# Optimization experiments

Measured on AMD Instinct MI355X. Metric: run time of the kernel, lower is better.

The kernel has to match this reference:

```python
import jax, jax.numpy as jnp
import numpy as np

HID, INTER, DK = 768, 1536, 128
NEG_INF = 1.0e12
LOG512 = float(np.log(512.0))


def setup_inputs() -> dict:
    key = jax.random.key(0)
    k1, k2, k3 = jax.random.split(key, 3)
    B, S = 4, 2048
    hidden_states = jax.random.normal(k1, (B, S, HID), dtype=jnp.float32)
    attention_mask = jnp.ones((B, S), dtype=jnp.int32)
    # i_dense: hidden -> 2*INTER + DK (no bias); o_dense: INTER -> hidden (no bias)
    Wi = jax.random.normal(k2, (HID, 2 * INTER + DK), dtype=jnp.float32) * (HID ** -0.5)
    Wo = jax.random.normal(k3, (INTER, HID), dtype=jnp.float32) * (INTER ** -0.5)
    q_gamma = jnp.ones((DK,), dtype=jnp.float32)  # ScaleOffset scale, offset=False
    k_gamma = jnp.ones((DK,), dtype=jnp.float32)
    return {"hidden_states": hidden_states, "Wi": Wi, "Wo": Wo,
            "q_gamma": q_gamma, "k_gamma": k_gamma,
            "attention_mask": attention_mask}


def reference(hidden_states, Wi, Wo, q_gamma, k_gamma, attention_mask):
    # i_dense + swish, then split into u, v, qk
    x = jax.nn.silu(jnp.einsum('bsh,ho->bso', hidden_states, Wi))
    u = x[..., :INTER]
    v = x[..., INTER:2 * INTER]
    qk = x[..., 2 * INTER:]
    q = qk * q_gamma
    k = qk * k_gamma
    # single-head attention scores
    a = jnp.einsum('bmd,bnd->bmn', q, k) / (DK ** 0.5)
    mask = attention_mask[:, None, :]  # [B,1,N]
    a = jnp.where(mask == 0, -NEG_INF, a)
    l = jnp.sum(attention_mask, axis=-1, keepdims=True)[:, :, None].astype(a.dtype)  # [B,1,1]
    # softmax_plus: softmax(a * log(l) / log(512))
    A = jax.nn.softmax(a * jnp.log(l) / LOG512, axis=-1)
    # dropout inactive in eval mode
    o = jnp.einsum('bmi,ih->bmh', u * jnp.einsum('bmn,bnd->bmd', A, v), Wo)
    return o
```

## Files before the change

### kernel.cpp

```cpp
#include <hip/hip_runtime.h>
#include <hip/hip_bf16.h>
#include <math.h>

#define BATCH 4
#define SEQ   2048
#define HID   768
#define INTER 1536
#define DK    128
#define NTOT  3200
#define NTOTP 3328
#define MROWS 8192
#define LN512 6.2383246250395075f

typedef _Float16 half8   __attribute__((ext_vector_type(8)));
typedef _Float16 half4   __attribute__((ext_vector_type(4)));
typedef float    floatx4 __attribute__((ext_vector_type(4)));
typedef float    floatx16 __attribute__((ext_vector_type(16)));

typedef const __attribute__((address_space(1))) unsigned int* gas1_t;
typedef __attribute__((address_space(3))) unsigned int* las3_t;

static __device__ __forceinline__ void load16(const _Float16* g, _Float16* l) {
    __builtin_amdgcn_global_load_lds((gas1_t)g, (las3_t)l, 16, 0, 0);
}
#define WAIT_VM(N)    asm volatile("s_waitcnt vmcnt(" #N ")" ::: "memory")
#define WAIT_LGKM0()  asm volatile("s_waitcnt lgkmcnt(0)" ::: "memory")
#define BARRIER_RAW() asm volatile("s_barrier" ::: "memory")
#define GLOAD16(dst, ptr) \
    asm volatile("global_load_dwordx4 %0, %1, off" : "=v"(dst) : "v"(ptr) : "memory")

__global__ __launch_bounds__(256) void prep_kernel(
    const float* __restrict__ H, _Float16* __restrict__ Hb,
    const float* __restrict__ Wi, _Float16* __restrict__ WiT,
    const float* __restrict__ Wo, _Float16* __restrict__ WoT,
    const int* __restrict__ mask, float* __restrict__ scales)
{
    __shared__ _Float16 tile[32][33];
    __shared__ int sh[256];
    const int bid = blockIdx.x, tid = threadIdx.x;
    if (bid < 3072) {
        const int i = (bid * 256 + tid) * 8;
        float4 a = *reinterpret_cast<const float4*>(H + i);
        float4 b = *reinterpret_cast<const float4*>(H + i + 4);
        half8 h = {(_Float16)a.x, (_Float16)a.y, (_Float16)a.z, (_Float16)a.w,
                   (_Float16)b.x, (_Float16)b.y, (_Float16)b.z, (_Float16)b.w};
        *reinterpret_cast<half8*>(Hb + i) = h;
    } else if (bid < 3072 + 2496) {
        const int l = bid - 3072;
        const int c0 = (l % 104) * 32, r0 = (l / 104) * 32;
        const int tx = tid & 31, ty = tid >> 5;
#pragma unroll
        for (int j = 0; j < 32; j += 8)
            tile[tx][ty + j] = (c0 + tx < NTOT)
                ? (_Float16)Wi[(size_t)(r0 + ty + j) * NTOT + c0 + tx]
                : (_Float16)0.0f;
        __syncthreads();
#pragma unroll
        for (int j = 0; j < 32; j += 8)
            WiT[(size_t)(c0 + ty + j) * HID + r0 + tx] = tile[ty + j][tx];
    } else if (bid < 3072 + 2496 + 1152) {
        const int l = bid - (3072 + 2496);
        const int c0 = (l % 24) * 32, r0 = (l / 24) * 32;
        const int tx = tid & 31, ty = tid >> 5;
#pragma unroll
        for (int j = 0; j < 32; j += 8)
            tile[tx][ty + j] = (_Float16)Wo[(size_t)(r0 + ty + j) * HID + c0 + tx];
        __syncthreads();
#pragma unroll
        for (int j = 0; j < 32; j += 8)
            WoT[(size_t)(c0 + ty + j) * INTER + r0 + tx] = tile[ty + j][tx];
    } else {
        const int b = bid - (3072 + 2496 + 1152);
        int s = 0;
        for (int i = tid; i < SEQ; i += 256) s += mask[b * SEQ + i];
        sh[tid] = s;
        __syncthreads();
        for (int off = 128; off > 0; off >>= 1) {
            if (tid < off) sh[tid] += sh[tid + off];
            __syncthreads();
        }
        if (tid == 0) scales[b] = logf((float)sh[0]) / LN512;
    }
}

struct TileCtx {
    int tid, wave, lane, quad, l16, l31, half, wm, wn, c0, c1;
};
static __device__ __forceinline__ TileCtx make_ctx() {
    TileCtx t;
    t.tid = threadIdx.x;
    t.wave = t.tid >> 6; t.lane = t.tid & 63;
    t.quad = t.lane >> 4; t.l16 = t.lane & 15;
    t.l31 = t.lane & 31;  t.half = t.lane >> 5;
    t.wm = (t.wave & 1) * 64;
    t.wn = (t.wave >> 1) * 64;
    t.c0 = t.tid;
    t.c1 = t.tid + 256;
    return t;
}

static __device__ __forceinline__ void gemm_mainloop_3s32(
    const TileCtx& t,
    const _Float16* __restrict__ Ag, int lda,
    const _Float16* __restrict__ Bg, int ldb,
    int K, _Float16* smem, floatx16 acc[2][2])
{
    const int r0i = t.c0 >> 2, s0 = (((r0i >> 1) ^ (r0i >> 3)) & 3);
    const int r1i = t.c1 >> 2, s1 = (((r1i >> 1) ^ (r1i >> 3)) & 3);
    const int ak0 = ((t.c0 & 3) ^ s0) * 8;
    const int ak1 = ((t.c1 & 3) ^ s1) * 8;
    const _Float16* a0 = Ag + (size_t)r0i * lda + ak0;
    const _Float16* a1 = Ag + (size_t)r1i * lda + ak1;
    const _Float16* b0 = Bg + (size_t)r0i * ldb + ak0;
    const _Float16* b1 = Bg + (size_t)r1i * ldb + ak1;
    _Float16* Asl = smem + t.c0 * 8;
    _Float16* Bsl = smem + 12288 + t.c0 * 8;
    const int nIter = K >> 5;

    const int fsw = ((t.l31 >> 1) ^ (t.l31 >> 3)) & 3;

    load16(a0, Asl);        load16(a1, Asl + 2048);
    load16(b0, Bsl);        load16(b1, Bsl + 2048);
    if (nIter > 1) {
        load16(a0 + 32, Asl + 4096); load16(a1 + 32, Asl + 6144);
        load16(b0 + 32, Bsl + 4096); load16(b1 + 32, Bsl + 6144);
    }

    int sc = 0, sp = 2;
    for (int k = 0; k < nIter; ++k) {
        if (k + 1 < nIter) { WAIT_VM(4); } else { WAIT_VM(0); }
        BARRIER_RAW();
        if (k + 2 < nIter) {
            const int off = sp * 4096;
            const int k0 = (k + 2) << 5;
            load16(a0 + k0, Asl + off); load16(a1 + k0, Asl + off + 2048);
            load16(b0 + k0, Bsl + off); load16(b1 + k0, Bsl + off + 2048);
        }
        const _Float16* Ab = smem + sc * 4096;
        const _Float16* Bb = smem + 12288 + sc * 4096;
        half8 af[2][2], bf[2][2];
#pragma unroll
        for (int mt = 0; mt < 2; ++mt)
#pragma unroll
            for (int h = 0; h < 2; ++h)
                af[mt][h] = *reinterpret_cast<const half8*>(
                    Ab + (t.wm + mt * 32 + t.l31) * 32 + (((h * 2 + t.half) ^ fsw) * 8));
#pragma unroll
        for (int nt = 0; nt < 2; ++nt)
#pragma unroll
            for (int h = 0; h < 2; ++h)
                bf[nt][h] = *reinterpret_cast<const half8*>(
                    Bb + (t.wn + nt * 32 + t.l31) * 32 + (((h * 2 + t.half) ^ fsw) * 8));
#pragma unroll
        for (int h = 0; h < 2; ++h)
#pragma unroll
            for (int mt = 0; mt < 2; ++mt)
#pragma unroll
                for (int nt = 0; nt < 2; ++nt)
                    acc[mt][nt] = __builtin_amdgcn_mfma_f32_32x32x16_f16(af[mt][h], bf[nt][h], acc[mt][nt], 0, 0, 0);
        WAIT_LGKM0();
        sc = (sc == 2) ? 0 : sc + 1;
        sp = (sp == 2) ? 0 : sp + 1;
    }
}

__global__ __launch_bounds__(512, 2) void gemm1_kernel(
    const _Float16* __restrict__ Hb, const _Float16* __restrict__ WiT,
    const float* __restrict__ qg, const float* __restrict__ kg,
    _Float16* __restrict__ u, _Float16* __restrict__ vT,
    _Float16* __restrict__ q, _Float16* __restrict__ k)
{
    __shared__ _Float16 smem[65536];
    const int tid = threadIdx.x;
    const int lane = tid & 63, wave = tid >> 6;
    const int quad = lane >> 4, l16 = lane & 15;
    const int wm = wave >> 2, wn = wave & 3;

    const int f = blockIdx.x;
    const int xcd = f & 7, i = f >> 3;
    const int m0 = (xcd * 4 + (i & 3)) * 256;
    const int ntile = i >> 2;
    const int n0 = ntile * 256;

    const _Float16* Ag = Hb  + (size_t)m0 * HID;
    const _Float16* Bg = WiT + (size_t)n0 * HID;

    const int rA = tid >> 2;
    const int csw = ((tid & 3) ^ ((rA >> 1) & 3)) * 8;
    const _Float16* pa0 = Ag + (size_t)rA * HID + csw;
    const _Float16* pa1 = pa0 + (size_t)128 * HID;
    const _Float16* pb0 = Bg + (size_t)rA * HID + csw;
    const _Float16* pb1 = pb0 + (size_t)128 * HID;

    const int sw8 = (l16 >> 1) & 3;
    const int qs  = (quad ^ sw8) * 8;
    const int aoff = (wm * 128 + l16) * 32 + qs;
    const int boff = 8192 + (wn * 64 + l16) * 32 + qs;

    floatx4 acc[8][4] = {};

    const int nKt = HID / 32;

#pragma unroll
    for (int pt = 0; pt < 3; ++pt) {
        _Float16* ld = smem + pt * 16384 + tid * 8;
        const int ko = pt * 32;
        load16(pa0 + ko, ld);
        load16(pa1 + ko, ld + 4096);
        load16(pb0 + ko, ld + 8192);
        load16(pb1 + ko, ld + 12288);
    }
    WAIT_VM(8);
    BARRIER_RAW();

    for (int t = 0; t < nKt; ++t) {
        const _Float16* sl = smem + (t & 3) * 16384;
        if (t + 3 < nKt) {
            _Float16* ld = smem + ((t + 3) & 3) * 16384 + tid * 8;
            const int ko = (t + 3) * 32;
            load16(pa0 + ko, ld);        load16(pa1 + ko, ld + 4096);
            load16(pb0 + ko, ld + 8192); load16(pb1 + ko, ld + 12288);
        }
        half8 af[8], bf[4];
#pragma unroll
        for (int mt = 0; mt < 8; ++mt)
            af[mt] = *reinterpret_cast<const half8*>(sl + aoff + mt * 512);
#pragma unroll
        for (int nt = 0; nt < 4; ++nt)
            bf[nt] = *reinterpret_cast<const half8*>(sl + boff + nt * 512);
        __builtin_amdgcn_s_setprio(1);
#pragma unroll
        for (int mt = 0; mt < 8; ++mt)
#pragma unroll
            for (int nt = 0; nt < 4; ++nt)
                acc[mt][nt] = __builtin_amdgcn_mfma_f32_16x16x32_f16(af[mt], bf[nt], acc[mt][nt], 0, 0, 0);
        __builtin_amdgcn_s_setprio(0);
        if (t <= nKt - 4)      { WAIT_VM(8); }
        else if (t == nKt - 3) { WAIT_VM(4); }
        else if (t == nKt - 2) { WAIT_VM(0); }
        BARRIER_RAW();
    }
    __syncthreads();

    if (ntile < 6) {
#pragma unroll
        for (int mt = 0; mt < 8; ++mt) {
#pragma unroll
            for (int nt = 0; nt < 4; ++nt) {
                const int col = n0 + wn * 64 + nt * 16 + l16;
#pragma unroll
                for (int i2 = 0; i2 < 4; ++i2) {
                    const int row = m0 + wm * 128 + mt * 16 + quad * 4 + i2;
                    float x = acc[mt][nt][i2];
                    float y = x / (1.0f + __expf(-x));
                    u[(size_t)row * INTER + col] = (_Float16)y;
                }
            }
        }
    } else if (ntile < 12) {
        const int bb = m0 >> 11, sloc = m0 & (SEQ - 1), cI = n0 - INTER;
#pragma unroll
        for (int mt = 0; mt < 8; ++mt) {
#pragma unroll
            for (int nt = 0; nt < 4; ++nt) {
                const int cl  = wn * 64 + nt * 16 + l16;
                const int rl0 = wm * 128 + mt * 16 + quad * 4;
                half4 pk;
#pragma unroll
                for (int i2 = 0; i2 < 4; ++i2) {
                    float x = acc[mt][nt][i2];
                    pk[i2] = (_Float16)(x / (1.0f + __expf(-x)));
                }
                *reinterpret_cast<half4*>(smem + cl * 256 + (rl0 ^ ((cl & 31) << 3))) = pk;
            }
        }
        __syncthreads();
#pragma unroll
        for (int p = 0; p < 16; ++p) {
            const int chunk = p * 512 + tid;
            const int cl = chunk >> 5, scn = chunk & 31;
            half8 v = *reinterpret_cast<const half8*>(smem + cl * 256 + ((scn ^ (cl & 31)) << 3));
            *reinterpret_cast<half8*>(vT + ((size_t)bb * INTER + cI + cl) * SEQ + sloc + scn * 8) = v;
        }
    } else {
        if (wn < 2) {
#pragma unroll
            for (int mt = 0; mt < 8; ++mt) {
#pragma unroll
                for (int nt = 0; nt < 4; ++nt) {
                    const int cq = wn * 64 + nt * 16 + l16;
                    const float qgv = qg[cq], kgv = kg[cq];
#pragma unroll
                    for (int i2 = 0; i2 < 4; ++i2) {
                        const int row = m0 + wm * 128 + mt * 16 + quad * 4 + i2;
                        float x = acc[mt][nt][i2];
                        float y = x / (1.0f + __expf(-x));
                        q[(size_t)row * DK + cq] = (_Float16)(y * qgv);
                        k[(size_t)row * DK + cq] = (_Float16)(y * kgv);
                    }
                }
            }
        }
    }
}

__global__ __launch_bounds__(256) void scores_kernel(
    const _Float16* __restrict__ q, const _Float16* __restrict__ k,
    const int* __restrict__ mask, const float* __restrict__ scales,
    _Float16* __restrict__ P)
{
    __shared__ _Float16 ps[16 * 2056];
    __shared__ float redmax[4][16];
    __shared__ float redsum[4][16];
    const int f = blockIdx.x;
    const int xcd = f & 7, i = f >> 3;
    const int b = xcd >> 1;
    const int m0 = ((xcd & 1) * 64 + i) * 16;
    const int tid = threadIdx.x;
    const int wave = tid >> 6, lane = tid & 63, quad = lane >> 4, l16 = lane & 15;
    const float scale = scales[b];

    half8 aq[4];
    const _Float16* qrow = q + (b * SEQ + m0 + l16) * DK + quad * 8;
#pragma unroll
    for (int kk = 0; kk < 4; ++kk) aq[kk] = *reinterpret_cast<const half8*>(qrow + kk * 32);

    floatx4 sc[32];
#pragma unroll
    for (int nt = 0; nt < 32; ++nt) {
        int n0 = nt * 64 + wave * 16;
        const _Float16* krow = k + (b * SEQ + n0 + l16) * DK + quad * 8;
        floatx4 acc = {};
#pragma unroll
        for (int kk = 0; kk < 4; ++kk) {
            half8 bq = *reinterpret_cast<const half8*>(krow + kk * 32);
            acc = __builtin_amdgcn_mfma_f32_16x16x32_f16(aq[kk], bq, acc, 0, 0, 0);
        }
        sc[nt] = acc;
    }

    const float rs = 0.08838834764831845f * scale;
    const float mval = -1e12f * scale;
    float rmax[4] = {-3.4e38f, -3.4e38f, -3.4e38f, -3.4e38f};
#pragma unroll
    for (int nt = 0; nt < 32; ++nt) {
        int ncol = nt * 64 + wave * 16 + l16;
        bool mok = mask[b * SEQ + ncol] != 0;
#pragma unroll
        for (int i2 = 0; i2 < 4; ++i2) {
            float s = mok ? sc[nt][i2] * rs : mval;
            sc[nt][i2] = s;
            rmax[i2] = fmaxf(rmax[i2], s);
        }
    }
#pragma unroll
    for (int i2 = 0; i2 < 4; ++i2) {
#pragma unroll
        for (int off = 1; off < 16; off <<= 1)
            rmax[i2] = fmaxf(rmax[i2], __shfl_xor(rmax[i2], off, 64));
    }
    if (l16 == 0) {
#pragma unroll
        for (int i2 = 0; i2 < 4; ++i2) redmax[wave][quad * 4 + i2] = rmax[i2];
    }
    __syncthreads();
#pragma unroll
    for (int i2 = 0; i2 < 4; ++i2) {
        int r = quad * 4 + i2;
        rmax[i2] = fmaxf(fmaxf(redmax[0][r], redmax[1][r]), fmaxf(redmax[2][r], redmax[3][r]));
    }
    float rsum[4] = {0.f, 0.f, 0.f, 0.f};
#pragma unroll
    for (int nt = 0; nt < 32; ++nt) {
#pragma unroll
        for (int i2 = 0; i2 < 4; ++i2) {
            float e = __expf(sc[nt][i2] - rmax[i2]);
            sc[nt][i2] = e;
            rsum[i2] += e;
        }
    }
#pragma unroll
    for (int i2 = 0; i2 < 4; ++i2) {
#pragma unroll
        for (int off = 1; off < 16; off <<= 1) rsum[i2] += __shfl_xor(rsum[i2], off, 64);
    }
    if (l16 == 0) {
#pragma unroll
        for (int i2 = 0; i2 < 4; ++i2) redsum[wave][quad * 4 + i2] = rsum[i2];
    }
    __syncthreads();
#pragma unroll
    for (int i2 = 0; i2 < 4; ++i2) {
        int r = quad * 4 + i2;
        float tot = redsum[0][r] + redsum[1][r] + redsum[2][r] + redsum[3][r];
        float inv = 1.0f / tot;
#pragma unroll
        for (int nt = 0; nt < 32; ++nt) {
            int ncol = nt * 64 + wave * 16 + l16;
            ps[r * 2056 + ncol] = (_Float16)(sc[nt][i2] * inv);
        }
    }
    __syncthreads();
    _Float16* Pfb = P + (size_t)b * SEQ * SEQ;
#pragma unroll
    for (int p = 0; p < 16; ++p) {
        const int chunk = p * 256 + tid;
        const int row = chunk & 15, c8 = chunk >> 4;
        half8 v = *reinterpret_cast<const half8*>(ps + row * 2056 + c8 * 8);
        *reinterpret_cast<half8*>(Pfb + ((size_t)c8 * SEQ + m0 + row) * 8) = v;
    }
}

__global__ __launch_bounds__(256) void pv_kernel(
    const _Float16* __restrict__ Pf, const _Float16* __restrict__ vT,
    _Float16* __restrict__ u)
{
    __shared__ _Float16 smem[16384];
    TileCtx t = make_ctx();
    const int f = blockIdx.x;
    const int xcd = f & 7, i = f >> 3;
    const int b = i / 24, j = i % 24;
    const int m0 = (xcd * 2 + (j & 1)) * 128;
    const int n0 = (j >> 1) * 128;
    const _Float16* Pfb = Pf + (size_t)b * SEQ * SEQ;
    const _Float16* vTb = vT + (size_t)b * INTER * SEQ;

    const int r0i = t.c0 >> 2, s0 = (((r0i >> 1) ^ (r0i >> 3)) & 3);
    const int r1i = t.c1 >> 2, s1 = (((r1i >> 1) ^ (r1i >> 3)) & 3);
    const _Float16* b0 = vTb + (size_t)(n0 + r0i) * SEQ + ((t.c0 & 3) ^ s0) * 8;
    const _Float16* b1 = vTb + (size_t)(n0 + r1i) * SEQ + ((t.c1 & 3) ^ s1) * 8;
    const int fsw = ((t.l31 >> 1) ^ (t.l31 >> 3)) & 3;

    const _Float16* pA0 = Pfb + (size_t)t.half * (SEQ * 8)
                        + (size_t)(m0 + t.wm + t.l31) * 8;
    const _Float16* pA1 = pA0 + 32 * 8;

    floatx16 acc[2][2] = {};
    half8 afA[2][2], afB[2][2], bfA[2][2], bfB[2][2];

#define PV_GLOADA(AF, K) do {                                                  \
        const size_t co_ = (size_t)(K) * 4 * (SEQ * 8);                        \
        GLOAD16(AF[0][0], pA0 + co_);                                          \
        GLOAD16(AF[0][1], pA0 + co_ + 2 * (SEQ * 8));                          \
        GLOAD16(AF[1][0], pA1 + co_);                                          \
        GLOAD16(AF[1][1], pA1 + co_ + 2 * (SEQ * 8));                          \
    } while (0)

#define PV_STAGEB(K) do {                                                      \
        _Float16* ld_ = smem + ((K) & 3) * 4096 + t.c0 * 8;                    \
        const int ko_ = (K) << 5;                                              \
        load16(b0 + ko_, ld_);                                                 \
        load16(b1 + ko_, ld_ + 2048);                                          \
    } while (0)

#define PV_READB(BF, SLOT) do {                                                \
        const _Float16* Bb_ = smem + (SLOT) * 4096;                            \
        _Pragma("unroll")                                                      \
        for (int nt = 0; nt < 2; ++nt)                                         \
            _Pragma("unroll")                                                  \
            for (int h = 0; h < 2; ++h)                                        \
                BF[nt][h] = *reinterpret_cast<const half8*>(                   \
                    Bb_ + (t.wn + nt * 32 + t.l31) * 32 + (((h * 2 + t.half) ^ fsw) * 8)); \
    } while (0)

#define PV_ITER(K, AFC, BFC, AFN, BFN) do {                                    \
        if ((K) + 1 < 64) PV_GLOADA(AFN, (K) + 1);                             \
        if ((K) + 2 < 64) PV_STAGEB((K) + 2);                                  \
        if ((K) + 2 < 64)      { WAIT_VM(6); }                                 \
        else if ((K) + 1 < 64) { WAIT_VM(4); }                                 \
        else                   { WAIT_VM(0); }                                 \
        __builtin_amdgcn_sched_barrier(0);                                     \
        BARRIER_RAW();                                                         \
        if ((K) + 1 < 64) PV_READB(BFN, ((K) + 1) & 3);                        \
        __builtin_amdgcn_s_setprio(1);                                         \
        _Pragma("unroll")                                                      \
        for (int h = 0; h < 2; ++h)                                            \
            _Pragma("unroll")                                                  \
            for (int mt = 0; mt < 2; ++mt)                                     \
                _Pragma("unroll")                                              \
                for (int nt = 0; nt < 2; ++nt)                                 \
                    acc[mt][nt] = __builtin_amdgcn_mfma_f32_32x32x16_f16(      \
                        AFC[mt][h], BFC[nt][h], acc[mt][nt], 0, 0, 0);         \
        __builtin_amdgcn_s_setprio(0);                                         \
        WAIT_LGKM0();                                                          \
    } while (0)

    PV_STAGEB(0);
    PV_STAGEB(1);
    PV_GLOADA(afA, 0);
    WAIT_VM(6);
    BARRIER_RAW();
    PV_READB(bfA, 0);

    for (int k = 0; k < 64; k += 2) {
        PV_ITER(k,     afA, bfA, afB, bfB);
        PV_ITER(k + 1, afB, bfB, afA, bfA);
    }

#pragma unroll
    for (int mt = 0; mt < 2; ++mt) {
#pragma unroll
        for (int nt = 0; nt < 2; ++nt) {
            int col = n0 + t.wn + nt * 32 + t.l31;
#pragma unroll
            for (int reg = 0; reg < 16; ++reg) {
                int row = m0 + t.wm + mt * 32 + (reg & 3) + 8 * (reg >> 2) + 4 * t.half;
                size_t gidx = ((size_t)(b * SEQ + row)) * INTER + col;
                float uv = (float)u[gidx];
                u[gidx] = (_Float16)(acc[mt][nt][reg] * uv);
            }
        }
    }
}

__global__ __launch_bounds__(256) void gemm2_kernel(
    const _Float16* __restrict__ tin, const _Float16* __restrict__ WoT,
    float* __restrict__ out)
{
    __shared__ _Float16 smem[24576];
    TileCtx t = make_ctx();
    const int f = blockIdx.x;
    const int xcd = f & 7, i = f >> 3;
    const int m0 = ((xcd << 3) | (i & 7)) * 128;
    const int n0 = (i >> 3) * 128;

    floatx16 acc[2][2] = {};
    gemm_mainloop_3s32(t, tin + (size_t)m0 * INTER, INTER, WoT + (size_t)n0 * INTER, INTER, INTER, smem, acc);

#pragma unroll
    for (int mt = 0; mt < 2; ++mt) {
#pragma unroll
        for (int nt = 0; nt < 2; ++nt) {
            int col = n0 + t.wn + nt * 32 + t.l31;
#pragma unroll
            for (int reg = 0; reg < 16; ++reg) {
                int row = m0 + t.wm + mt * 32 + (reg & 3) + 8 * (reg >> 2) + 4 * t.half;
                out[(size_t)row * HID + col] = acc[mt][nt][reg];
            }
        }
    }
}

extern "C" void kernel_launch(void* const* d_in, const int* in_sizes, int n_in,
                              void* d_out, int out_size, void* d_ws, size_t ws_size,
                              hipStream_t stream) {
    const float* H    = (const float*)d_in[0];
    const float* Wi   = (const float*)d_in[1];
    const float* Wo   = (const float*)d_in[2];
    const float* qg   = (const float*)d_in[3];
    const float* kg   = (const float*)d_in[4];
    const int*   mask = (const int*)d_in[5];
    float* out = (float*)d_out;

    char* base = (char*)d_ws;
    size_t off = 0;
    auto alloc = [&](size_t bytes) { void* p = base + off; off = (off + bytes + 255) & ~(size_t)255; return p; };
    _Float16* Hb   = (_Float16*)alloc((size_t)MROWS * HID * 2);
    _Float16* WiT  = (_Float16*)alloc((size_t)NTOTP * HID * 2);
    _Float16* WoT  = (_Float16*)alloc((size_t)HID * INTER * 2);
    _Float16* u    = (_Float16*)alloc((size_t)MROWS * INTER * 2);
    _Float16* vT   = (_Float16*)alloc((size_t)BATCH * INTER * SEQ * 2);
    _Float16* q    = (_Float16*)alloc((size_t)MROWS * DK * 2);
    _Float16* k    = (_Float16*)alloc((size_t)MROWS * DK * 2);
    _Float16* P    = (_Float16*)alloc((size_t)BATCH * SEQ * SEQ * 2);
    float*    scales = (float*)alloc(4 * sizeof(float));

    prep_kernel<<<6724, 256, 0, stream>>>(H, Hb, Wi, WiT, Wo, WoT, mask, scales);
    gemm1_kernel<<<416, 512, 0, stream>>>(Hb, WiT, qg, kg, u, vT, q, k);
    scores_kernel<<<512, 256, 0, stream>>>(q, k, mask, scales, P);
    pv_kernel<<<768, 256, 0, stream>>>(P, vT, u);
    gemm2_kernel<<<384, 256, 0, stream>>>(u, WoT, out);
}
```

Measured before the change: 297.7 us.

## Retile output GEMM to 64x128 blocks with reordered triple-buffered pipeline

Replaces the shared 128x128 GEMM mainloop for the output projection with a dedicated 64x128 tile kernel, doubling the grid to 768 blocks and raising occupancy via launch_bounds(256,4) and smaller LDS. The loop now reads fragments, issues the next stage's loads, then synchronizes once before MFMAs, with setprio raised around the MFMA block. The aim is to fill more CUs (384 blocks underfilled the GPU) and hide latency, at the cost of less A/B reuse per block.

New measurement: 301.8 us. No clear change (+1.4%).

```diff
diff --git a/kernel.cpp b/kernel.cpp
--- a/kernel.cpp
+++ b/kernel.cpp
@@ -97,71 +97,6 @@
     t.c0 = t.tid;
     t.c1 = t.tid + 256;
     return t;
-}
-
-static __device__ __forceinline__ void gemm_mainloop_3s32(
-    const TileCtx& t,
-    const _Float16* __restrict__ Ag, int lda,
-    const _Float16* __restrict__ Bg, int ldb,
-    int K, _Float16* smem, floatx16 acc[2][2])
-{
-    const int r0i = t.c0 >> 2, s0 = (((r0i >> 1) ^ (r0i >> 3)) & 3);
-    const int r1i = t.c1 >> 2, s1 = (((r1i >> 1) ^ (r1i >> 3)) & 3);
-    const int ak0 = ((t.c0 & 3) ^ s0) * 8;
-    const int ak1 = ((t.c1 & 3) ^ s1) * 8;
-    const _Float16* a0 = Ag + (size_t)r0i * lda + ak0;
-    const _Float16* a1 = Ag + (size_t)r1i * lda + ak1;
-    const _Float16* b0 = Bg + (size_t)r0i * ldb + ak0;
-    const _Float16* b1 = Bg + (size_t)r1i * ldb + ak1;
-    _Float16* Asl = smem + t.c0 * 8;
-    _Float16* Bsl = smem + 12288 + t.c0 * 8;
-    const int nIter = K >> 5;
-
-    const int fsw = ((t.l31 >> 1) ^ (t.l31 >> 3)) & 3;
-
-    load16(a0, Asl);        load16(a1, Asl + 2048);
-    load16(b0, Bsl);        load16(b1, Bsl + 2048);
-    if (nIter > 1) {
-        load16(a0 + 32, Asl + 4096); load16(a1 + 32, Asl + 6144);
-        load16(b0 + 32, Bsl + 4096); load16(b1 + 32, Bsl + 6144);
-    }
-
-    int sc = 0, sp = 2;
-    for (int k = 0; k < nIter; ++k) {
-        if (k + 1 < nIter) { WAIT_VM(4); } else { WAIT_VM(0); }
-        BARRIER_RAW();
-        if (k + 2 < nIter) {
-            const int off = sp * 4096;
-            const int k0 = (k + 2) << 5;
-            load16(a0 + k0, Asl + off); load16(a1 + k0, Asl + off + 2048);
-            load16(b0 + k0, Bsl + off); load16(b1 + k0, Bsl + off + 2048);
-        }
-        const _Float16* Ab = smem + sc * 4096;
-        const _Float16* Bb = smem + 12288 + sc * 4096;
-        half8 af[2][2], bf[2][2];
-#pragma unroll
-        for (int mt = 0; mt < 2; ++mt)
-#pragma unroll
-            for (int h = 0; h < 2; ++h)
-                af[mt][h] = *reinterpret_cast<const half8*>(
-                    Ab + (t.wm + mt * 32 + t.l31) * 32 + (((h * 2 + t.half) ^ fsw) * 8));
-#pragma unroll
-        for (int nt = 0; nt < 2; ++nt)
-#pragma unroll
-            for (int h = 0; h < 2; ++h)
-                bf[nt][h] = *reinterpret_cast<const half8*>(
-                    Bb + (t.wn + nt * 32 + t.l31) * 32 + (((h * 2 + t.half) ^ fsw) * 8));
-#pragma unroll
-        for (int h = 0; h < 2; ++h)
-#pragma unroll
-            for (int mt = 0; mt < 2; ++mt)
-#pragma unroll
-                for (int nt = 0; nt < 2; ++nt)
-                    acc[mt][nt] = __builtin_amdgcn_mfma_f32_32x32x16_f16(af[mt][h], bf[nt][h], acc[mt][nt], 0, 0, 0);
-        WAIT_LGKM0();
-        sc = (sc == 2) ? 0 : sc + 1;
-        sp = (sp == 2) ? 0 : sp + 1;
-    }
 }
 
 __global__ __launch_bounds__(512, 2) void gemm1_kernel(
@@ -513,30 +448,77 @@
     }
 }
 
-__global__ __launch_bounds__(256) void gemm2_kernel(
+__global__ __launch_bounds__(256, 4) void gemm2_kernel(
     const _Float16* __restrict__ tin, const _Float16* __restrict__ WoT,
     float* __restrict__ out)
 {
-    __shared__ _Float16 smem[24576];
-    TileCtx t = make_ctx();
+    __shared__ _Float16 smem[18432];
+    const int tid = threadIdx.x;
+    const int lane = tid & 63, wave = tid >> 6;
+    const int l31 = lane & 31, half = lane >> 5;
     const int f = blockIdx.x;
     const int xcd = f & 7, i = f >> 3;
-    const int m0 = ((xcd << 3) | (i & 7)) * 128;
-    const int n0 = (i >> 3) * 128;
-
-    floatx16 acc[2][2] = {};
-    gemm_mainloop_3s32(t, tin + (size_t)m0 * INTER, INTER, WoT + (size_t)n0 * INTER, INTER, INTER, smem, acc);
+    const int m0 = (xcd * 16 + (i & 15)) * 64;
+    const int n0 = (i >> 4) * 128;
+
+    const int rS = tid >> 2;
+    const int csw = ((tid & 3) ^ (((rS >> 1) ^ (rS >> 3)) & 3)) * 8;
+    const _Float16* a0 = tin + (size_t)(m0 + rS) * INTER + csw;
+    const _Float16* b0 = WoT + (size_t)(n0 + rS) * INTER + csw;
+    const _Float16* b1 = b0 + (size_t)64 * INTER;
+
+    const int fsw = ((l31 >> 1) ^ (l31 >> 3)) & 3;
+    floatx16 acc[2] = {};
+    const int nIter = INTER >> 5;
+
+#define G2_STAGE(KK) do {                                                      \
+        _Float16* sl_ = smem + ((KK) % 3) * 6144;                              \
+        const int ko_ = (KK) << 5;                                             \
+        load16(a0 + ko_, sl_ + tid * 8);                                       \
+        load16(b0 + ko_, sl_ + 2048 + tid * 8);                                \
+        load16(b1 + ko_, sl_ + 4096 + tid * 8);                                \
+    } while (0)
+
+    G2_STAGE(0);
+    G2_STAGE(1);
+    WAIT_VM(3);
+    BARRIER_RAW();
+
+    for (int k = 0; k < nIter; ++k) {
+        const _Float16* sl = smem + (k % 3) * 6144;
+        half8 af[2][2], bf[2];
+#pragma unroll
+        for (int mt = 0; mt < 2; ++mt)
+#pragma unroll
+            for (int h = 0; h < 2; ++h)
+                af[mt][h] = *reinterpret_cast<const half8*>(
+                    sl + (mt * 32 + l31) * 32 + (((h * 2 + half) ^ fsw) * 8));
+#pragma unroll
+        for (int h = 0; h < 2; ++h)
+            bf[h] = *reinterpret_cast<const half8*>(
+                sl + 2048 + (wave * 32 + l31) * 32 + (((h * 2 + half) ^ fsw) * 8));
+        if (k + 2 < nIter) G2_STAGE(k + 2);
+        if (k + 2 < nIter) { WAIT_VM(3); } else { WAIT_VM(0); }
+        WAIT_LGKM0();
+        __builtin_amdgcn_sched_barrier(0);
+        BARRIER_RAW();
+        __builtin_amdgcn_s_setprio(1);
+#pragma unroll
+        for (int h = 0; h < 2; ++h)
+#pragma unroll
+            for (int mt = 0; mt < 2; ++mt)
+                acc[mt] = __builtin_amdgcn_mfma_f32_32x32x16_f16(
+                    af[mt][h], bf[h], acc[mt], 0, 0, 0);
+        __builtin_amdgcn_s_setprio(0);
+    }
 
 #pragma unroll
     for (int mt = 0; mt < 2; ++mt) {
-#pragma unroll
-        for (int nt = 0; nt < 2; ++nt) {
-            int col = n0 + t.wn + nt * 32 + t.l31;
-#pragma unroll
-            for (int reg = 0; reg < 16; ++reg) {
-                int row = m0 + t.wm + mt * 32 + (reg & 3) + 8 * (reg >> 2) + 4 * t.half;
-                out[(size_t)row * HID + col] = acc[mt][nt][reg];
-            }
+        const int col = n0 + wave * 32 + l31;
+#pragma unroll
+        for (int reg = 0; reg < 16; ++reg) {
+            const int row = m0 + mt * 32 + (reg & 3) + 8 * (reg >> 2) + 4 * half;
+            out[(size_t)row * HID + col] = acc[mt][reg];
         }
     }
 }
@@ -569,5 +551,5 @@
     gemm1_kernel<<<416, 512, 0, stream>>>(Hb, WiT, qg, kg, u, vT, q, k);
     scores_kernel<<<512, 256, 0, stream>>>(q, k, mask, scales, P);
     pv_kernel<<<768, 256, 0, stream>>>(P, vT, u);
-    gemm2_kernel<<<384, 256, 0, stream>>>(u, WoT, out);
-}
+    gemm2_kernel<<<768, 256, 0, stream>>>(u, WoT, out);
+}
```
